# Kernel tuning notes

Hardware: AMD Instinct MI355X
Metric: run time of the kernel (lower is better)

## Reference

```python
import jax, jax.numpy as jnp
import numpy as np

N_NODES = 50000
N_EDGES = 800000
N_GRAPHS = 256
D_FEAT = 96
HIDDEN = 32


def setup_inputs() -> dict:
    key = jax.random.key(0)
    ks = jax.random.split(key, 8)
    x = jax.random.normal(ks[0], (N_NODES, D_FEAT), dtype=jnp.float32)
    edge_index = jax.random.randint(ks[1], (2, N_EDGES), 0, N_NODES, dtype=jnp.int64)
    batch = jnp.sort(jax.random.randint(ks[2], (N_NODES,), 0, N_GRAPHS, dtype=jnp.int64))
    W1 = jax.random.normal(ks[3], (D_FEAT, HIDDEN), dtype=jnp.float32) * 0.05
    b1 = jnp.zeros((HIDDEN,), dtype=jnp.float32)
    W2 = jax.random.normal(ks[4], (HIDDEN, HIDDEN), dtype=jnp.float32) * 0.05
    b2 = jnp.zeros((HIDDEN,), dtype=jnp.float32)
    Wc = jax.random.normal(ks[5], (HIDDEN, 2), dtype=jnp.float32) * 0.05
    bc = jnp.zeros((2,), dtype=jnp.float32)
    return {"x": x, "edge_index": edge_index, "batch": batch,
            "W1": W1, "b1": b1, "W2": W2, "b2": b2, "Wc": Wc, "bc": bc}


def reference(x, edge_index, batch, W1, b1, W2, b2, Wc, bc):
    src, dst = edge_index[0], edge_index[1]
    # GIN aggregation (eps=0): h_i = x_i + sum_{j -> i} x_j, scatter-add over edges
    agg = jax.ops.segment_sum(x[src], dst, num_segments=N_NODES)
    h = agg + x
    # 2-layer MLP inside GINConv
    h = jnp.maximum(h @ W1 + b1, 0.0) @ W2 + b2
    # outer ReLU (F.relu in forward)
    h = jnp.maximum(h, 0.0)
    # global mean pool per graph
    sums = jax.ops.segment_sum(h, batch, num_segments=N_GRAPHS)          # [G, H]
    counts = jax.ops.segment_sum(jnp.ones((N_NODES,), h.dtype), batch,
                                 num_segments=N_GRAPHS)                   # [G]
    pooled = sums / jnp.maximum(counts, 1.0)[:, None]
    return pooled @ Wc + bc  # [G, 2]
```

## Files before the change

kernel.cpp:

```cpp
#include <hip/hip_runtime.h>
#include <hip/hip_fp16.h>

#define N_NODES 50000
#define N_EDGES 800000
#define N_GRAPHS 256
#define D_FEAT 96
#define HIDDEN 32

#define NB 782
#define BN 64
#define PB 500
#define PCHUNK 1600
#define SEGCAP 16
#define NLOAD 8
#define GWIN 4
#define LCAP2 2048
#define XT 64
#define XBLK 782
#define XS_STRIDE 97
#define DUMMY_NODE N_NODES

__global__ void __launch_bounds__(256)
k_front(const float* __restrict__ x, const float* __restrict__ W1,
        __half* __restrict__ y16,
        const int* __restrict__ src, const int* __restrict__ dst,
        unsigned int* __restrict__ binned, unsigned short* __restrict__ cnt,
        float* __restrict__ sums, float* __restrict__ counts) {
    __shared__ __align__(16) char smem[26656];
    int blk = blockIdx.x;
    int tid = threadIdx.x;
    if (blk < PB) {
        int* hcur = (int*)smem;
        for (int i = tid; i < NB; i += 256) hcur[i] = 0;
        __syncthreads();

        int e0 = blk * PCHUNK, e1 = e0 + PCHUNK;
        for (int it = 0; it < PCHUNK; it += 1024) {
            int e = e0 + it + tid * 4;
            if (e < e1) {
                int4 s4 = *(const int4*)&src[e];
                int4 d4 = *(const int4*)&dst[e];
                unsigned w0 = (unsigned)s4.x | ((unsigned)(d4.x & 255) << 16);
                unsigned w1 = (unsigned)s4.y | ((unsigned)(d4.y & 255) << 16);
                unsigned w2 = (unsigned)s4.z | ((unsigned)(d4.z & 255) << 16);
                unsigned w3 = (unsigned)s4.w | ((unsigned)(d4.w & 255) << 16);
                int b0 = d4.x >> 6, b1 = d4.y >> 6, b2 = d4.z >> 6, b3 = d4.w >> 6;
                int p0 = atomicAdd(&hcur[b0], 1);
                int p1 = atomicAdd(&hcur[b1], 1);
                int p2 = atomicAdd(&hcur[b2], 1);
                int p3 = atomicAdd(&hcur[b3], 1);
                if (p0 < SEGCAP) binned[((size_t)b0 * PB + blk) * SEGCAP + p0] = w0;
                if (p1 < SEGCAP) binned[((size_t)b1 * PB + blk) * SEGCAP + p1] = w1;
                if (p2 < SEGCAP) binned[((size_t)b2 * PB + blk) * SEGCAP + p2] = w2;
                if (p3 < SEGCAP) binned[((size_t)b3 * PB + blk) * SEGCAP + p3] = w3;
            }
        }
        __syncthreads();

        for (int i = tid; i < NB; i += 256) {
            int c = hcur[i]; if (c > SEGCAP) c = SEGCAP;
            cnt[i * PB + blk] = (unsigned short)c;
        }
    } else {
        float* xs = (float*)smem;
        int xb = blk - PB;
        int n0 = xb * XT;
        int nn = N_NODES - n0; if (nn > XT) nn = XT;

        int gid = xb * 256 + tid;
        if (gid < N_GRAPHS * HIDDEN) sums[gid] = 0.f;
        if (gid < N_GRAPHS) counts[gid] = 0.f;
        if (xb == 0 && tid < HIDDEN)
            y16[(size_t)DUMMY_NODE * HIDDEN + tid] = __float2half(0.f);

        const float4* xsrc = (const float4*)(x + (size_t)n0 * D_FEAT);
        int nf4 = nn * (D_FEAT / 4);
        for (int idx = tid; idx < nf4; idx += 256) {
            int ln = (idx * 2731) >> 16;
            int k4 = idx - ln * 24;
            float4 v = xsrc[idx];
            float* dp = &xs[ln * XS_STRIDE + k4 * 4];
            dp[0] = v.x; dp[1] = v.y; dp[2] = v.z; dp[3] = v.w;
        }
        __syncthreads();

        int lane = tid & 63;
        int f0 = (tid >> 6) << 3;
        f0 = __builtin_amdgcn_readfirstlane(f0);

        if (lane < nn) {
            const float* xr = &xs[lane * XS_STRIDE];
            const float4* W1v = (const float4*)W1;
            float acc[8];
#pragma unroll
            for (int j = 0; j < 8; ++j) acc[j] = 0.f;
#pragma unroll
            for (int k = 0; k < D_FEAT; ++k) {
                float xv = xr[k];
                float4 wa = W1v[k * 8 + (f0 >> 2)];
                float4 wb = W1v[k * 8 + (f0 >> 2) + 1];
                acc[0] = fmaf(xv, wa.x, acc[0]);
                acc[1] = fmaf(xv, wa.y, acc[1]);
                acc[2] = fmaf(xv, wa.z, acc[2]);
                acc[3] = fmaf(xv, wa.w, acc[3]);
                acc[4] = fmaf(xv, wb.x, acc[4]);
                acc[5] = fmaf(xv, wb.y, acc[5]);
                acc[6] = fmaf(xv, wb.z, acc[6]);
                acc[7] = fmaf(xv, wb.w, acc[7]);
            }
            __half2 h01 = __floats2half2_rn(acc[0], acc[1]);
            __half2 h23 = __floats2half2_rn(acc[2], acc[3]);
            __half2 h45 = __floats2half2_rn(acc[4], acc[5]);
            __half2 h67 = __floats2half2_rn(acc[6], acc[7]);
            float4 pack;
            pack.x = __uint_as_float(*(const unsigned*)&h01);
            pack.y = __uint_as_float(*(const unsigned*)&h23);
            pack.z = __uint_as_float(*(const unsigned*)&h45);
            pack.w = __uint_as_float(*(const unsigned*)&h67);
            *(float4*)&y16[(size_t)(n0 + lane) * HIDDEN + f0] = pack;
        }
    }
}

__global__ void __launch_bounds__(1024)
k_agg(const unsigned int* __restrict__ binned, const unsigned short* __restrict__ cnt,
      const __half* __restrict__ y16, const int* __restrict__ batch,
      const float* __restrict__ b1, const float* __restrict__ W2,
      const float* __restrict__ b2,
      float* __restrict__ sums, float* __restrict__ counts) {
    __shared__ unsigned short list2[LCAP2];
    __shared__ unsigned short cs[512];
    __shared__ unsigned int ncnt[BN];
    __shared__ unsigned int offs[BN + 1];
    __shared__ unsigned int cur[BN];
    __shared__ float w2s[HIDDEN * HIDDEN];
    __shared__ float accs[GWIN * HIDDEN];
    __shared__ float cntsl[GWIN];

    int tid = threadIdx.x;
    int bin = blockIdx.x;

    if (tid < BN) ncnt[tid] = 0;
    w2s[tid] = W2[tid];
    if (tid < GWIN * HIDDEN) accs[tid] = 0.f;
    if (tid < GWIN) cntsl[tid] = 0.f;
    if (tid < 512)
        cs[tid] = (tid < PB) ? cnt[bin * PB + tid] : (unsigned short)0;

    const unsigned int* ebase = binned + (size_t)bin * PB * SEGCAP;
    unsigned u[NLOAD];
#pragma unroll
    for (int j = 0; j < NLOAD; ++j) {
        int idx = tid + j * 1024;
        u[j] = (idx < PB * SEGCAP) ? ebase[idx] : 0u;
    }
    __syncthreads();

#pragma unroll
    for (int j = 0; j < NLOAD; ++j) {
        int idx = tid + j * 1024;
        int s = idx >> 4;
        int i = idx & 15;
        if (i < (int)cs[s])
            atomicAdd(&ncnt[(u[j] >> 16) & 63], 1u);
    }
    __syncthreads();

    if (tid < BN) {
        unsigned pc = (ncnt[tid] + 7u) & ~7u;
        unsigned v = pc;
#pragma unroll
        for (int d = 1; d < BN; d <<= 1) {
            unsigned t = __shfl_up(v, d, 64);
            if (tid >= d) v += t;
        }
        offs[tid + 1] = v;
        cur[tid] = v - pc;
    }
    if (tid == 0) offs[0] = 0;
    __syncthreads();

#pragma unroll
    for (int j = 0; j < NLOAD; ++j) {
        int idx = tid + j * 1024;
        int s = idx >> 4;
        int i = idx & 15;
        if (i < (int)cs[s]) {
            unsigned p = u[j];
            unsigned pos = atomicAdd(&cur[(p >> 16) & 63], 1u);
            if (pos < LCAP2) list2[pos] = (unsigned short)(p & 0xFFFFu);
        }
    }
    __syncthreads();
    if (tid < BN) {
        unsigned i0 = cur[tid], i1 = offs[tid + 1];
        for (unsigned i = i0; i < i1 && i < LCAP2; ++i)
            list2[i] = (unsigned short)DUMMY_NODE;
    }
    __syncthreads();

    int node0 = bin << 6;
    int nn = N_NODES - node0; if (nn > BN) nn = BN;
    int g = tid >> 5;
    int f = tid & 31;
    int gfirst = batch[node0];

    for (int ln = g * 2; ln < g * 2 + 2; ++ln) {
        if (ln >= nn) break;
        int node = node0 + ln;
        float acc = __half2float(y16[(size_t)node * HIDDEN + f]);
        int j = offs[ln];
        int jend = offs[ln + 1]; if (jend > LCAP2) jend = LCAP2;
        for (; j < jend; j += 8) {
            ushort4 qa = *(const ushort4*)&list2[j];
            ushort4 qb = *(const ushort4*)&list2[j + 4];
            float a0 = __half2float(y16[(size_t)qa.x * HIDDEN + f]);
            float a1 = __half2float(y16[(size_t)qa.y * HIDDEN + f]);
            float a2 = __half2float(y16[(size_t)qa.z * HIDDEN + f]);
            float a3 = __half2float(y16[(size_t)qa.w * HIDDEN + f]);
            float a4 = __half2float(y16[(size_t)qb.x * HIDDEN + f]);
            float a5 = __half2float(y16[(size_t)qb.y * HIDDEN + f]);
            float a6 = __half2float(y16[(size_t)qb.z * HIDDEN + f]);
            float a7 = __half2float(y16[(size_t)qb.w * HIDDEN + f]);
            acc += ((a0 + a1) + (a2 + a3)) + ((a4 + a5) + (a6 + a7));
        }

        float h1 = fmaxf(acc + b1[f], 0.f);
        float h2 = b2[f];
#pragma unroll
        for (int k = 0; k < HIDDEN; ++k)
            h2 = fmaf(__shfl(h1, k, 32), w2s[k * HIDDEN + f], h2);
        float h = fmaxf(h2, 0.f);

        int gr = batch[node];
        int b = gr - gfirst;
        if (b < GWIN) {
            atomicAdd(&accs[b * HIDDEN + f], h);
            if (f == 0) atomicAdd(&cntsl[b], 1.f);
        } else {
            atomicAdd(&sums[(size_t)gr * HIDDEN + f], h);
            if (f == 0) atomicAdd(&counts[gr], 1.f);
        }
    }
    __syncthreads();

    if (tid < GWIN * HIDDEN) {
        float v = accs[tid];
        if (v != 0.f) atomicAdd(&sums[(size_t)gfirst * HIDDEN + tid], v);
    }
    if (tid < GWIN) {
        float c = cntsl[tid];
        if (c != 0.f) atomicAdd(&counts[gfirst + tid], c);
    }
}

__global__ void k_out(const float* __restrict__ sums, const float* __restrict__ counts,
                      const float* __restrict__ Wc, const float* __restrict__ bc,
                      float* __restrict__ out) {
    int g = threadIdx.x;
    if (g >= N_GRAPHS) return;
    float inv = 1.f / fmaxf(counts[g], 1.f);
    float o0 = bc[0], o1 = bc[1];
#pragma unroll
    for (int k = 0; k < HIDDEN; ++k) {
        float p = sums[(size_t)g * HIDDEN + k] * inv;
        o0 = fmaf(p, Wc[k * 2 + 0], o0);
        o1 = fmaf(p, Wc[k * 2 + 1], o1);
    }
    out[g * 2 + 0] = o0;
    out[g * 2 + 1] = o1;
}

extern "C" void kernel_launch(void* const* d_in, const int* in_sizes, int n_in,
                              void* d_out, int out_size, void* d_ws, size_t ws_size,
                              hipStream_t stream) {
    const float* x     = (const float*)d_in[0];
    const int*   ei    = (const int*)d_in[1];
    const int*   batch = (const int*)d_in[2];
    const float* W1    = (const float*)d_in[3];
    const float* b1    = (const float*)d_in[4];
    const float* W2    = (const float*)d_in[5];
    const float* b2    = (const float*)d_in[6];
    const float* Wc    = (const float*)d_in[7];
    const float* bc    = (const float*)d_in[8];
    float* out = (float*)d_out;

    char* ws = (char*)d_ws;
    float*          sums   = (float*)ws;
    float*          counts = (float*)(ws + 32768);
    unsigned short* cnt    = (unsigned short*)(ws + 33792);
    unsigned int*   binned = (unsigned int*)(ws + 815792);
    __half*         y16    = (__half*)(ws + 25839792);

    k_front<<<PB + XBLK, 256, 0, stream>>>(
        x, W1, y16, ei, ei + N_EDGES, binned, cnt, sums, counts);

    k_agg<<<NB, 1024, 0, stream>>>(binned, cnt, y16, batch,
                                   b1, W2, b2, sums, counts);

    k_out<<<1, 256, 0, stream>>>(sums, counts, Wc, bc, out);
}
```

Before: 140.0 us.

## Double destination bin size to 128 nodes and stage W1 in LDS

Destination bins now hold 128 nodes instead of 64, with half as many partition blocks, twice the edge chunk and segment capacity, and a two-wavefront prefix scan over the bin counts. The aggregation kernel launches half as many blocks, and each thread group handles four nodes. The MLP front-end now copies W1 into shared memory instead of reading it from global memory in the inner loop. This is meant to cut the size of the binned buffer and per-bin overhead, but it gives the aggregation stage fewer blocks to spread across the GPU and raises shared-memory use per block.

```diff
diff --git a/kernel.cpp b/kernel.cpp
--- a/kernel.cpp
+++ b/kernel.cpp
@@ -7,14 +7,14 @@
 #define D_FEAT 96
 #define HIDDEN 32
 
-#define NB 782
-#define BN 64
-#define PB 500
-#define PCHUNK 1600
-#define SEGCAP 16
+#define NB 391
+#define BN 128
+#define PB 250
+#define PCHUNK 3200
+#define SEGCAP 32
 #define NLOAD 8
 #define GWIN 4
-#define LCAP2 2048
+#define LCAP2 3456
 #define XT 64
 #define XBLK 782
 #define XS_STRIDE 97
@@ -26,7 +26,7 @@
         const int* __restrict__ src, const int* __restrict__ dst,
         unsigned int* __restrict__ binned, unsigned short* __restrict__ cnt,
         float* __restrict__ sums, float* __restrict__ counts) {
-    __shared__ __align__(16) char smem[26656];
+    __shared__ __align__(16) char smem[37120];
     int blk = blockIdx.x;
     int tid = threadIdx.x;
     if (blk < PB) {
@@ -40,11 +40,11 @@
             if (e < e1) {
                 int4 s4 = *(const int4*)&src[e];
                 int4 d4 = *(const int4*)&dst[e];
-                unsigned w0 = (unsigned)s4.x | ((unsigned)(d4.x & 255) << 16);
-                unsigned w1 = (unsigned)s4.y | ((unsigned)(d4.y & 255) << 16);
-                unsigned w2 = (unsigned)s4.z | ((unsigned)(d4.z & 255) << 16);
-                unsigned w3 = (unsigned)s4.w | ((unsigned)(d4.w & 255) << 16);
-                int b0 = d4.x >> 6, b1 = d4.y >> 6, b2 = d4.z >> 6, b3 = d4.w >> 6;
+                unsigned w0 = (unsigned)s4.x | ((unsigned)(d4.x & 127) << 16);
+                unsigned w1 = (unsigned)s4.y | ((unsigned)(d4.y & 127) << 16);
+                unsigned w2 = (unsigned)s4.z | ((unsigned)(d4.z & 127) << 16);
+                unsigned w3 = (unsigned)s4.w | ((unsigned)(d4.w & 127) << 16);
+                int b0 = d4.x >> 7, b1 = d4.y >> 7, b2 = d4.z >> 7, b3 = d4.w >> 7;
                 int p0 = atomicAdd(&hcur[b0], 1);
                 int p1 = atomicAdd(&hcur[b1], 1);
                 int p2 = atomicAdd(&hcur[b2], 1);
@@ -62,7 +62,8 @@
             cnt[i * PB + blk] = (unsigned short)c;
         }
     } else {
-        float* xs = (float*)smem;
+        float* xs  = (float*)smem;
+        float* w1s = (float*)(smem + 24832);
         int xb = blk - PB;
         int n0 = xb * XT;
         int nn = N_NODES - n0; if (nn > XT) nn = XT;
@@ -72,6 +73,9 @@
         if (gid < N_GRAPHS) counts[gid] = 0.f;
         if (xb == 0 && tid < HIDDEN)
             y16[(size_t)DUMMY_NODE * HIDDEN + tid] = __float2half(0.f);
+
+        for (int i = tid; i < (D_FEAT * HIDDEN) / 4; i += 256)
+            ((float4*)w1s)[i] = ((const float4*)W1)[i];
 
         const float4* xsrc = (const float4*)(x + (size_t)n0 * D_FEAT);
         int nf4 = nn * (D_FEAT / 4);
@@ -90,15 +94,14 @@
 
         if (lane < nn) {
             const float* xr = &xs[lane * XS_STRIDE];
-            const float4* W1v = (const float4*)W1;
             float acc[8];
 #pragma unroll
             for (int j = 0; j < 8; ++j) acc[j] = 0.f;
 #pragma unroll
             for (int k = 0; k < D_FEAT; ++k) {
                 float xv = xr[k];
-                float4 wa = W1v[k * 8 + (f0 >> 2)];
-                float4 wb = W1v[k * 8 + (f0 >> 2) + 1];
+                float4 wa = *(const float4*)&w1s[k * HIDDEN + f0];
+                float4 wb = *(const float4*)&w1s[k * HIDDEN + f0 + 4];
                 acc[0] = fmaf(xv, wa.x, acc[0]);
                 acc[1] = fmaf(xv, wa.y, acc[1]);
                 acc[2] = fmaf(xv, wa.z, acc[2]);
@@ -129,10 +132,11 @@
       const float* __restrict__ b2,
       float* __restrict__ sums, float* __restrict__ counts) {
     __shared__ unsigned short list2[LCAP2];
-    __shared__ unsigned short cs[512];
+    __shared__ unsigned short cs[256];
     __shared__ unsigned int ncnt[BN];
     __shared__ unsigned int offs[BN + 1];
     __shared__ unsigned int cur[BN];
+    __shared__ unsigned int wtot;
     __shared__ float w2s[HIDDEN * HIDDEN];
     __shared__ float accs[GWIN * HIDDEN];
     __shared__ float cntsl[GWIN];
@@ -144,7 +148,7 @@
     w2s[tid] = W2[tid];
     if (tid < GWIN * HIDDEN) accs[tid] = 0.f;
     if (tid < GWIN) cntsl[tid] = 0.f;
-    if (tid < 512)
+    if (tid < 256)
         cs[tid] = (tid < PB) ? cnt[bin * PB + tid] : (unsigned short)0;
 
     const unsigned int* ebase = binned + (size_t)bin * PB * SEGCAP;
@@ -159,21 +163,27 @@
 #pragma unroll
     for (int j = 0; j < NLOAD; ++j) {
         int idx = tid + j * 1024;
-        int s = idx >> 4;
-        int i = idx & 15;
-        if (i < (int)cs[s])
-            atomicAdd(&ncnt[(u[j] >> 16) & 63], 1u);
-    }
-    __syncthreads();
-
+        int s = idx >> 5;
+        int i = idx & 31;
+        if (idx < PB * SEGCAP && i < (int)cs[s])
+            atomicAdd(&ncnt[u[j] >> 16], 1u);
+    }
+    __syncthreads();
+
+    unsigned v = 0, pc = 0;
     if (tid < BN) {
-        unsigned pc = (ncnt[tid] + 7u) & ~7u;
-        unsigned v = pc;
-#pragma unroll
-        for (int d = 1; d < BN; d <<= 1) {
+        pc = (ncnt[tid] + 7u) & ~7u;
+        v = pc;
+#pragma unroll
+        for (int d = 1; d < 64; d <<= 1) {
             unsigned t = __shfl_up(v, d, 64);
-            if (tid >= d) v += t;
-        }
+            if ((tid & 63) >= d) v += t;
+        }
+        if (tid == 63) wtot = v;
+    }
+    __syncthreads();
+    if (tid < BN) {
+        if (tid >= 64) v += wtot;
         offs[tid + 1] = v;
         cur[tid] = v - pc;
     }
@@ -183,11 +193,11 @@
 #pragma unroll
     for (int j = 0; j < NLOAD; ++j) {
         int idx = tid + j * 1024;
-        int s = idx >> 4;
-        int i = idx & 15;
-        if (i < (int)cs[s]) {
+        int s = idx >> 5;
+        int i = idx & 31;
+        if (idx < PB * SEGCAP && i < (int)cs[s]) {
             unsigned p = u[j];
-            unsigned pos = atomicAdd(&cur[(p >> 16) & 63], 1u);
+            unsigned pos = atomicAdd(&cur[p >> 16], 1u);
             if (pos < LCAP2) list2[pos] = (unsigned short)(p & 0xFFFFu);
         }
     }
@@ -199,13 +209,13 @@
     }
     __syncthreads();
 
-    int node0 = bin << 6;
+    int node0 = bin << 7;
     int nn = N_NODES - node0; if (nn > BN) nn = BN;
     int g = tid >> 5;
     int f = tid & 31;
     int gfirst = batch[node0];
 
-    for (int ln = g * 2; ln < g * 2 + 2; ++ln) {
+    for (int ln = g * 4; ln < g * 4 + 4; ++ln) {
         if (ln >= nn) break;
         int node = node0 + ln;
         float acc = __half2float(y16[(size_t)node * HIDDEN + f]);
@@ -245,8 +255,8 @@
     __syncthreads();
 
     if (tid < GWIN * HIDDEN) {
-        float v = accs[tid];
-        if (v != 0.f) atomicAdd(&sums[(size_t)gfirst * HIDDEN + tid], v);
+        float vv = accs[tid];
+        if (vv != 0.f) atomicAdd(&sums[(size_t)gfirst * HIDDEN + tid], vv);
     }
     if (tid < GWIN) {
         float c = cntsl[tid];
@@ -289,8 +299,8 @@
     float*          sums   = (float*)ws;
     float*          counts = (float*)(ws + 32768);
     unsigned short* cnt    = (unsigned short*)(ws + 33792);
-    unsigned int*   binned = (unsigned int*)(ws + 815792);
-    __half*         y16    = (__half*)(ws + 25839792);
+    unsigned int*   binned = (unsigned int*)(ws + 229296);
+    __half*         y16    = (__half*)(ws + 12741296);
 
     k_front<<<PB + XBLK, 256, 0, stream>>>(
         x, W1, y16, ei, ei + N_EDGES, binned, cnt, sums, counts);
```

New measurement: 133.4 us. -4.7%, faster.
